# Kernel optimization log

Measured on AMD Instinct MI355X. Metric: run time of the kernel, lower is better.

Reference implementation:

```python
import jax, jax.numpy as jnp
import numpy as np

N = 50000
E = 600000
D = 128
BN_EPS = 1e-5


def _gcn_layer(x, src, dst, ew, W, b, n):
    # x: [N, Din] -> [N, Dout]; PyG GCNConv: linear, symmetric norm (self-loops
    # already appended to src/dst/ew by caller), gather, scatter-add, bias.
    h = x @ W  # [N, Dout]
    deg = jax.ops.segment_sum(ew, dst, num_segments=n)  # [N]
    dinv = jnp.where(deg > 0, jax.lax.rsqrt(jnp.maximum(deg, 1e-30)), 0.0)
    norm = dinv[src] * ew * dinv[dst]  # [E+N]
    msg = h[src] * norm[:, None]  # [E+N, Dout] -- dominant memory traffic
    out = jax.ops.segment_sum(msg, dst, num_segments=n)
    return out + b


def _bn_eval(x, gamma, beta, mean, var):
    return (x - mean) * jax.lax.rsqrt(var + BN_EPS) * gamma + beta


def setup_inputs() -> dict:
    key = jax.random.key(0)
    ks = jax.random.split(key, 16)
    s = 1.0 / np.sqrt(D)
    inp = {
        "x": jax.random.normal(ks[0], (N, D), dtype=jnp.float32),
        "edge_index": jax.random.randint(ks[1], (2, E), 0, N, dtype=jnp.int32),
        "edge_weight": jax.random.uniform(ks[2], (E,), dtype=jnp.float32),
        "W0": jax.random.uniform(ks[3], (D, D), jnp.float32, -s, s),
        "b0": jnp.zeros((D,), jnp.float32),
        "W1": jax.random.uniform(ks[4], (D, D), jnp.float32, -s, s),
        "b1": jnp.zeros((D,), jnp.float32),
        "gamma0": jnp.ones((D,), jnp.float32),
        "beta0": jnp.zeros((D,), jnp.float32),
        "mean0": 0.1 * jax.random.normal(ks[5], (D,), jnp.float32),
        "var0": jax.random.uniform(ks[6], (D,), jnp.float32, 0.5, 1.5),
        "gamma1": jnp.ones((D,), jnp.float32),
        "beta1": jnp.zeros((D,), jnp.float32),
        "mean1": 0.1 * jax.random.normal(ks[7], (D,), jnp.float32),
        "var1": jax.random.uniform(ks[8], (D,), jnp.float32, 0.5, 1.5),
        "act_params": jnp.ones((2,), jnp.float32),  # activation_params init = ones(num_layers)
    }
    return inp


def reference(x, edge_index, edge_weight, W0, b0, W1, b1, gamma0, beta0, mean0, var0, gamma1, beta1, mean1, var1, act_params):
    # Add self-loops with weight 1 (PyG gcn_norm fill_value=1), shared by both layers.
    loop = jnp.arange(N, dtype=edge_index.dtype)
    src = jnp.concatenate([edge_index[0], loop])
    dst = jnp.concatenate([edge_index[1], loop])
    ew = jnp.concatenate([edge_weight, jnp.ones((N,), edge_weight.dtype)])

    # layer 0: conv -> BN (eval: running stats) -> adaptive ReLU/GELU blend
    h = _gcn_layer(x, src, dst, ew, W0, b0, N)
    h = _bn_eval(h, gamma0, beta0, mean0, var0)
    alpha = jax.nn.sigmoid(act_params[0])
    h = alpha * jax.nn.relu(h) + (1.0 - alpha) * jax.nn.gelu(h, approximate=False)
    # dropout: identity in eval mode

    # layer 1 (last): conv -> BN, no activation/dropout
    h = _gcn_layer(h, src, dst, ew, W1, b1, N)
    h = _bn_eval(h, gamma1, beta1, mean1, var1)
    return h
```

## Files before the change

### kernel.cpp

```cpp
#include <hip/hip_runtime.h>
#include <hip/hip_fp16.h>
#include <math.h>
#include <type_traits>

#define D 128
#define BN_EPS 1e-5f
#define BCAP 64
#define FIX_SCALE 268435456.0f
#define FIX_INV   (1.0f / 268435456.0f)

typedef _Float16 half8 __attribute__((ext_vector_type(8)));
typedef float f32x4 __attribute__((ext_vector_type(4)));

__global__ void k_init(uint4* __restrict__ z, int n4,
                       const float* __restrict__ W0, const float* __restrict__ W1,
                       _Float16* __restrict__ p0, _Float16* __restrict__ p1, int Z) {
  if ((int)blockIdx.x < Z) {
    int i = blockIdx.x * 256 + threadIdx.x;
    if (i < n4) z[i] = make_uint4(0u, 0u, 0u, 0u);
    return;
  }
  const float* W = (blockIdx.x - Z) ? W1 : W0;
  _Float16* P = (blockIdx.x - Z) ? p1 : p0;
  for (int idx = threadIdx.x; idx < 32 * 64; idx += 256) {
    int ntks = idx >> 6;
    int lane = idx & 63;
    int nt = ntks >> 2, ks = ntks & 3;
    int kb = ks * 32 + (lane >> 4) * 8;
    int c = nt * 16 + (lane & 15);
#pragma unroll
    for (int i = 0; i < 8; ++i)
      P[(size_t)idx * 8 + i] = (_Float16)W[(size_t)(kb + i) * D + c];
  }
}

__global__ __launch_bounds__(256) void k_cnt_gemm0(const float* __restrict__ X,
                                                   const _Float16* __restrict__ Bp,
                                                   __half* __restrict__ H,
                                                   const int* __restrict__ dst,
                                                   const float* __restrict__ ew,
                                                   unsigned long long* cnt8,
                                                   int* __restrict__ rank,
                                                   int n, int e, int Gg) {
  if ((int)blockIdx.x >= Gg) {
    int base = ((int)blockIdx.x - Gg) * 2048 + threadIdx.x;
#pragma unroll
    for (int jj = 0; jj < 8; ++jj) {
      int i = base + jj * 256;
      if (i < e) {
        unsigned long long add = (1ull << 40) |
            (unsigned long long)(ew[i] * FIX_SCALE);
        unsigned long long old = atomicAdd(&cnt8[(size_t)dst[i] * 8], add);
        rank[i] = (int)(old >> 40);
      }
    }
    return;
  }

  const int lane = threadIdx.x & 63;
  const int wave = threadIdx.x >> 6;
  const int r0 = blockIdx.x * 64 + wave * 16;
  const int arow = r0 + (lane & 15);
  const int kbase = (lane >> 4) * 8;
  const bool av = arow < n;

  f32x4 acc[8];
#pragma unroll
  for (int t = 0; t < 8; ++t) acc[t] = (f32x4){0.f, 0.f, 0.f, 0.f};

#pragma unroll
  for (int ks = 0; ks < 4; ++ks) {
    half8 a;
    if (av) {
      const float* ap = X + (size_t)arow * D + ks * 32 + kbase;
      float4 f0 = *(const float4*)ap;
      float4 f1 = *(const float4*)(ap + 4);
      a[0] = (_Float16)f0.x; a[1] = (_Float16)f0.y;
      a[2] = (_Float16)f0.z; a[3] = (_Float16)f0.w;
      a[4] = (_Float16)f1.x; a[5] = (_Float16)f1.y;
      a[6] = (_Float16)f1.z; a[7] = (_Float16)f1.w;
    } else {
#pragma unroll
      for (int i = 0; i < 8; ++i) a[i] = (_Float16)0.f;
    }
#pragma unroll
    for (int nt = 0; nt < 8; ++nt) {
      half8 b = *(const half8*)(Bp + ((size_t)(nt * 4 + ks) * 64 + lane) * 8);
      acc[nt] = __builtin_amdgcn_mfma_f32_16x16x32_f16(a, b, acc[nt], 0, 0, 0);
    }
  }

  const int rbase = (lane >> 4) * 4;
  const int col = lane & 15;
#pragma unroll
  for (int nt = 0; nt < 8; ++nt) {
#pragma unroll
    for (int j = 0; j < 4; ++j) {
      int rr = r0 + rbase + j;
      if (rr < n) H[(size_t)rr * D + nt * 16 + col] = __float2half(acc[nt][j]);
    }
  }
}

__global__ void k_dinv2(const unsigned long long* __restrict__ cnt8,
                        int* __restrict__ cnt, float* __restrict__ dinv, int n) {
  int g = blockIdx.x * blockDim.x + threadIdx.x;
  if (g < n) {
    unsigned long long pv = cnt8[(size_t)g * 8];
    cnt[g] = (int)(pv >> 40);
    float ewsum = (float)(pv & 0xFFFFFFFFFFull) * FIX_INV;
    dinv[g] = rsqrtf(1.0f + ewsum);
  }
}

__global__ void k_bucket(const int* __restrict__ src, const int* __restrict__ dst,
                         const float* __restrict__ ew,
                         const int* __restrict__ rank, const float* __restrict__ dinv,
                         unsigned* __restrict__ pack4, int e) {
  int i = blockIdx.x * blockDim.x + threadIdx.x;
  if (i < e) {
    int d = dst[i], s = src[i];
    size_t pos = (size_t)d * BCAP + rank[i];
    __half c = __float2half(dinv[s] * ew[i]);
    pack4[pos] = ((unsigned)s << 16) | (unsigned)__half_as_ushort(c);
  }
}

__device__ __forceinline__ void h8_to_f(const uint4& r, float* f) {
  const __half2* hp = (const __half2*)&r;
#pragma unroll
  for (int t = 0; t < 4; ++t) {
    float2 v = __half22float2(hp[t]);
    f[2 * t] = v.x; f[2 * t + 1] = v.y;
  }
}

template <bool ACT>
__device__ __forceinline__ void agg_node(const __half* __restrict__ H,
                                         const unsigned* __restrict__ bkt, int kcnt,
                                         const float* __restrict__ dinv,
                                         const float* __restrict__ bias,
                                         const float* __restrict__ gamma,
                                         const float* __restrict__ beta,
                                         const float* __restrict__ mean,
                                         const float* __restrict__ var,
                                         float alpha, int g, int q, int j, float* acc) {
#pragma unroll
  for (int t = 0; t < 8; ++t) acc[t] = 0.f;

  for (int kb = 0; kb < kcnt; kb += 16) {
    int m = kcnt - kb;
    if (m > 16) m = 16;
    unsigned pl = 0u;
    if (q < m) pl = bkt[kb + q];
#pragma unroll
    for (int t = 0; t < 16; ++t) {
      if (t < m) {
        unsigned pp = (unsigned)__shfl((int)pl, t, 16);
        float w = __half2float(__ushort_as_half((unsigned short)(pp & 0xffffu)));
        uint4 r = *(const uint4*)(H + (size_t)(pp >> 16) * D + j);
        float f[8];
        h8_to_f(r, f);
#pragma unroll
        for (int u = 0; u < 8; ++u) acc[u] += w * f[u];
      }
    }
  }

  float dg = dinv[g];
  uint4 rs = *(const uint4*)(H + (size_t)g * D + j);
  float fs[8];
  h8_to_f(rs, fs);
#pragma unroll
  for (int t = 0; t < 8; ++t) acc[t] = dg * acc[t] + dg * dg * fs[t];

  float bb[8], gm[8], bt[8], mn[8], vr[8];
  *(float4*)&bb[0] = *(const float4*)(bias + j);  *(float4*)&bb[4] = *(const float4*)(bias + j + 4);
  *(float4*)&gm[0] = *(const float4*)(gamma + j); *(float4*)&gm[4] = *(const float4*)(gamma + j + 4);
  *(float4*)&bt[0] = *(const float4*)(beta + j);  *(float4*)&bt[4] = *(const float4*)(beta + j + 4);
  *(float4*)&mn[0] = *(const float4*)(mean + j);  *(float4*)&mn[4] = *(const float4*)(mean + j + 4);
  *(float4*)&vr[0] = *(const float4*)(var + j);   *(float4*)&vr[4] = *(const float4*)(var + j + 4);

#pragma unroll
  for (int t = 0; t < 8; ++t) {
    float vv = (acc[t] + bb[t] - mn[t]) * rsqrtf(vr[t] + BN_EPS) * gm[t] + bt[t];
    if (ACT) {
      float rl = fmaxf(vv, 0.f);
      float ge = 0.5f * vv * (1.f + erff(vv * 0.70710678118654752f));
      vv = alpha * rl + (1.f - alpha) * ge;
    }
    acc[t] = vv;
  }
}

__global__ __launch_bounds__(256) void k_agg_gemm(const __half* __restrict__ H,
                                                  const int* __restrict__ cnt,
                                                  const unsigned* __restrict__ pack4,
                                                  const float* __restrict__ dinv,
                                                  const float* __restrict__ bias,
                                                  const float* __restrict__ gamma,
                                                  const float* __restrict__ beta,
                                                  const float* __restrict__ mean,
                                                  const float* __restrict__ var,
                                                  const float* __restrict__ act_params,
                                                  const _Float16* __restrict__ Bp,
                                                  __half* __restrict__ Hout, int n) {
  __shared__ _Float16 sA[16][136];
  const int tid = threadIdx.x;
  const int row0 = blockIdx.x * 16;
  const int grp = tid >> 4;
  const int q = tid & 15;
  const int j = q * 8;
  const float alpha = 1.f / (1.f + expf(-act_params[0]));

  const int g = row0 + grp;
  half8 st;
  if (g < n) {
    float acc[8];
    agg_node<true>(H, pack4 + (size_t)g * BCAP, cnt[g], dinv,
                   bias, gamma, beta, mean, var, alpha, g, q, j, acc);
#pragma unroll
    for (int t = 0; t < 8; ++t) st[t] = (_Float16)acc[t];
  } else {
#pragma unroll
    for (int t = 0; t < 8; ++t) st[t] = (_Float16)0.f;
  }
  *(half8*)&sA[grp][j] = st;
  __syncthreads();

  const int lane = tid & 63;
  const int wave = tid >> 6;
  const int ntb = wave * 2;
  const int arowl = lane & 15;
  const int kbase = (lane >> 4) * 8;

  f32x4 acc[2];
#pragma unroll
  for (int t = 0; t < 2; ++t) acc[t] = (f32x4){0.f, 0.f, 0.f, 0.f};

#pragma unroll
  for (int ks = 0; ks < 4; ++ks) {
    half8 a = *(const half8*)&sA[arowl][ks * 32 + kbase];
#pragma unroll
    for (int nt = 0; nt < 2; ++nt) {
      half8 b = *(const half8*)(Bp + ((size_t)((ntb + nt) * 4 + ks) * 64 + lane) * 8);
      acc[nt] = __builtin_amdgcn_mfma_f32_16x16x32_f16(a, b, acc[nt], 0, 0, 0);
    }
  }

  const int rbase = (lane >> 4) * 4;
  const int col = lane & 15;
#pragma unroll
  for (int nt = 0; nt < 2; ++nt) {
#pragma unroll
    for (int jj = 0; jj < 4; ++jj) {
      int rr = row0 + rbase + jj;
      if (rr < n) Hout[(size_t)rr * D + (ntb + nt) * 16 + col] = __float2half(acc[nt][jj]);
    }
  }
}

template <typename OutT, bool ACT>
__global__ __launch_bounds__(256) void k_agg(const __half* __restrict__ H,
                                             const int* __restrict__ cnt,
                                             const unsigned* __restrict__ pack4,
                                             const float* __restrict__ dinv,
                                             const float* __restrict__ bias,
                                             const float* __restrict__ gamma,
                                             const float* __restrict__ beta,
                                             const float* __restrict__ mean,
                                             const float* __restrict__ var,
                                             const float* __restrict__ act_params,
                                             OutT* __restrict__ out, int n) {
  int g = blockIdx.x * 16 + (threadIdx.x >> 4);
  if (g >= n) return;
  const int q = threadIdx.x & 15;
  const int j = q * 8;
  const float alpha = ACT ? 1.f / (1.f + expf(-act_params[0])) : 0.f;

  float acc[8];
  agg_node<ACT>(H, pack4 + (size_t)g * BCAP, cnt[g], dinv,
                bias, gamma, beta, mean, var, alpha, g, q, j, acc);

  if constexpr (std::is_same<OutT, __half>::value) {
    uint4 st;
    __half2* hp = (__half2*)&st;
    hp[0] = __floats2half2_rn(acc[0], acc[1]);
    hp[1] = __floats2half2_rn(acc[2], acc[3]);
    hp[2] = __floats2half2_rn(acc[4], acc[5]);
    hp[3] = __floats2half2_rn(acc[6], acc[7]);
    *(uint4*)(out + (size_t)g * D + j) = st;
  } else {
    *(float4*)(out + (size_t)g * D + j)     = make_float4(acc[0], acc[1], acc[2], acc[3]);
    *(float4*)(out + (size_t)g * D + j + 4) = make_float4(acc[4], acc[5], acc[6], acc[7]);
  }
}

extern "C" void kernel_launch(void* const* d_in, const int* in_sizes, int n_in,
                              void* d_out, int out_size, void* d_ws, size_t ws_size,
                              hipStream_t stream) {
  const float* x      = (const float*)d_in[0];
  const int*   ei     = (const int*)d_in[1];
  const float* ew     = (const float*)d_in[2];
  const float* W0     = (const float*)d_in[3];
  const float* b0     = (const float*)d_in[4];
  const float* W1     = (const float*)d_in[5];
  const float* b1     = (const float*)d_in[6];
  const float* gamma0 = (const float*)d_in[7];
  const float* beta0  = (const float*)d_in[8];
  const float* mean0  = (const float*)d_in[9];
  const float* var0   = (const float*)d_in[10];
  const float* gamma1 = (const float*)d_in[11];
  const float* beta1  = (const float*)d_in[12];
  const float* mean1  = (const float*)d_in[13];
  const float* var1   = (const float*)d_in[14];
  const float* act    = (const float*)d_in[15];

  const int n = in_sizes[0] / D;
  const int e = in_sizes[2];
  const int* srcp = ei;
  const int* dstp = ei + e;

  uintptr_t p = (uintptr_t)d_ws;
  auto carve = [&p](size_t bytes) -> void* {
    void* r = (void*)p;
    p += (bytes + 255) & ~(size_t)255;
    return r;
  };
  float*    dinv  = (float*)carve(sizeof(float) * n);
  int*      cnt   = (int*)carve(sizeof(int) * n);
  int*      rank  = (int*)carve(sizeof(int) * e);
  unsigned long long* cnt8 = (unsigned long long*)carve(sizeof(unsigned long long) * (size_t)n * 8);
  _Float16* w0p   = (_Float16*)carve(sizeof(_Float16) * 32 * 64 * 8);
  _Float16* w1p   = (_Float16*)carve(sizeof(_Float16) * 32 * 64 * 8);
  unsigned* pack4 = (unsigned*)carve(sizeof(unsigned) * (size_t)n * BCAP);
  __half*   h16   = (__half*)carve(sizeof(__half) * (size_t)n * D);
  __half*   h16b  = (__half*)carve(sizeof(__half) * (size_t)n * D);
  float*    out   = (float*)d_out;

  const int tpb = 256;
  const int nb_n = (n + tpb - 1) / tpb;
  const int nb_e = (e + tpb - 1) / tpb;
  const int Gc   = (e + 2047) / 2048;
  const int Gg   = (n + 63) / 64;
  const int nz4  = n * 4;
  const int Z    = (nz4 + tpb - 1) / tpb;

  k_init<<<Z + 2, tpb, 0, stream>>>((uint4*)cnt8, nz4, W0, W1, w0p, w1p, Z);
  k_cnt_gemm0<<<Gg + Gc, tpb, 0, stream>>>(x, w0p, h16, dstp, ew, cnt8, rank, n, e, Gg);
  k_dinv2<<<nb_n, tpb, 0, stream>>>(cnt8, cnt, dinv, n);
  k_bucket<<<nb_e, tpb, 0, stream>>>(srcp, dstp, ew, rank, dinv, pack4, e);

  k_agg_gemm<<<(n + 15) / 16, tpb, 0, stream>>>(
      h16, cnt, pack4, dinv, b0, gamma0, beta0, mean0, var0, act, w1p, h16b, n);

  k_agg<float, false><<<(n + 15) / 16, tpb, 0, stream>>>(
      h16b, cnt, pack4, dinv, b1, gamma1, beta1, mean1, var1, act, out, n);
}
```

Measured before the change: 119.6 us.

## Fuse edge bucketing into the counting atomic pass, deferring dinv[src] to aggregation

Edges are now written directly into per-destination buckets at the moment the atomic counter returns their rank. This removes the separate bucket kernel and the rank array. Because dinv is not yet known at that point, each bucket entry becomes 8 bytes (src, fp32 edge weight), and dinv[src] is gathered inside both aggregation kernels. The trade is one fewer launch and less rank traffic, against twice the bucket bytes and an extra random dinv gather per edge in each of the two aggregations.

```diff
diff --git a/kernel.cpp b/kernel.cpp
--- a/kernel.cpp
+++ b/kernel.cpp
@@ -34,24 +34,29 @@
   }
 }
 
-__global__ __launch_bounds__(256) void k_cnt_gemm0(const float* __restrict__ X,
-                                                   const _Float16* __restrict__ Bp,
-                                                   __half* __restrict__ H,
-                                                   const int* __restrict__ dst,
-                                                   const float* __restrict__ ew,
-                                                   unsigned long long* cnt8,
-                                                   int* __restrict__ rank,
-                                                   int n, int e, int Gg) {
+__global__ __launch_bounds__(256) void k_scat_gemm0(const float* __restrict__ X,
+                                                    const _Float16* __restrict__ Bp,
+                                                    __half* __restrict__ H,
+                                                    const int* __restrict__ src,
+                                                    const int* __restrict__ dst,
+                                                    const float* __restrict__ ew,
+                                                    unsigned long long* cnt8,
+                                                    uint2* __restrict__ pack8,
+                                                    int n, int e, int Gg) {
   if ((int)blockIdx.x >= Gg) {
     int base = ((int)blockIdx.x - Gg) * 2048 + threadIdx.x;
 #pragma unroll
     for (int jj = 0; jj < 8; ++jj) {
       int i = base + jj * 256;
       if (i < e) {
+        float w = ew[i];
+        int d = dst[i];
         unsigned long long add = (1ull << 40) |
-            (unsigned long long)(ew[i] * FIX_SCALE);
-        unsigned long long old = atomicAdd(&cnt8[(size_t)dst[i] * 8], add);
-        rank[i] = (int)(old >> 40);
+            (unsigned long long)(w * FIX_SCALE);
+        unsigned long long old = atomicAdd(&cnt8[(size_t)d * 8], add);
+        int rank = (int)(old >> 40);
+        pack8[(size_t)d * BCAP + rank] =
+            make_uint2((unsigned)src[i], __float_as_uint(w));
       }
     }
     return;
@@ -113,19 +118,6 @@
   }
 }
 
-__global__ void k_bucket(const int* __restrict__ src, const int* __restrict__ dst,
-                         const float* __restrict__ ew,
-                         const int* __restrict__ rank, const float* __restrict__ dinv,
-                         unsigned* __restrict__ pack4, int e) {
-  int i = blockIdx.x * blockDim.x + threadIdx.x;
-  if (i < e) {
-    int d = dst[i], s = src[i];
-    size_t pos = (size_t)d * BCAP + rank[i];
-    __half c = __float2half(dinv[s] * ew[i]);
-    pack4[pos] = ((unsigned)s << 16) | (unsigned)__half_as_ushort(c);
-  }
-}
-
 __device__ __forceinline__ void h8_to_f(const uint4& r, float* f) {
   const __half2* hp = (const __half2*)&r;
 #pragma unroll
@@ -137,7 +129,7 @@
 
 template <bool ACT>
 __device__ __forceinline__ void agg_node(const __half* __restrict__ H,
-                                         const unsigned* __restrict__ bkt, int kcnt,
+                                         const uint2* __restrict__ bkt, int kcnt,
                                          const float* __restrict__ dinv,
                                          const float* __restrict__ bias,
                                          const float* __restrict__ gamma,
@@ -151,14 +143,19 @@
   for (int kb = 0; kb < kcnt; kb += 16) {
     int m = kcnt - kb;
     if (m > 16) m = 16;
-    unsigned pl = 0u;
-    if (q < m) pl = bkt[kb + q];
+    unsigned sl = 0u;
+    float wl = 0.f;
+    if (q < m) {
+      uint2 pl = bkt[kb + q];
+      sl = pl.x;
+      wl = dinv[pl.x] * __uint_as_float(pl.y);
+    }
 #pragma unroll
     for (int t = 0; t < 16; ++t) {
       if (t < m) {
-        unsigned pp = (unsigned)__shfl((int)pl, t, 16);
-        float w = __half2float(__ushort_as_half((unsigned short)(pp & 0xffffu)));
-        uint4 r = *(const uint4*)(H + (size_t)(pp >> 16) * D + j);
+        unsigned s = (unsigned)__shfl((int)sl, t, 16);
+        float w = __shfl(wl, t, 16);
+        uint4 r = *(const uint4*)(H + (size_t)s * D + j);
         float f[8];
         h8_to_f(r, f);
 #pragma unroll
@@ -195,7 +192,7 @@
 
 __global__ __launch_bounds__(256) void k_agg_gemm(const __half* __restrict__ H,
                                                   const int* __restrict__ cnt,
-                                                  const unsigned* __restrict__ pack4,
+                                                  const uint2* __restrict__ pack8,
                                                   const float* __restrict__ dinv,
                                                   const float* __restrict__ bias,
                                                   const float* __restrict__ gamma,
@@ -217,7 +214,7 @@
   half8 st;
   if (g < n) {
     float acc[8];
-    agg_node<true>(H, pack4 + (size_t)g * BCAP, cnt[g], dinv,
+    agg_node<true>(H, pack8 + (size_t)g * BCAP, cnt[g], dinv,
                    bias, gamma, beta, mean, var, alpha, g, q, j, acc);
 #pragma unroll
     for (int t = 0; t < 8; ++t) st[t] = (_Float16)acc[t];
@@ -263,7 +260,7 @@
 template <typename OutT, bool ACT>
 __global__ __launch_bounds__(256) void k_agg(const __half* __restrict__ H,
                                              const int* __restrict__ cnt,
-                                             const unsigned* __restrict__ pack4,
+                                             const uint2* __restrict__ pack8,
                                              const float* __restrict__ dinv,
                                              const float* __restrict__ bias,
                                              const float* __restrict__ gamma,
@@ -279,7 +276,7 @@
   const float alpha = ACT ? 1.f / (1.f + expf(-act_params[0])) : 0.f;
 
   float acc[8];
-  agg_node<ACT>(H, pack4 + (size_t)g * BCAP, cnt[g], dinv,
+  agg_node<ACT>(H, pack8 + (size_t)g * BCAP, cnt[g], dinv,
                 bias, gamma, beta, mean, var, alpha, g, q, j, acc);
 
   if constexpr (std::is_same<OutT, __half>::value) {
@@ -329,31 +326,28 @@
   };
   float*    dinv  = (float*)carve(sizeof(float) * n);
   int*      cnt   = (int*)carve(sizeof(int) * n);
-  int*      rank  = (int*)carve(sizeof(int) * e);
   unsigned long long* cnt8 = (unsigned long long*)carve(sizeof(unsigned long long) * (size_t)n * 8);
   _Float16* w0p   = (_Float16*)carve(sizeof(_Float16) * 32 * 64 * 8);
   _Float16* w1p   = (_Float16*)carve(sizeof(_Float16) * 32 * 64 * 8);
-  unsigned* pack4 = (unsigned*)carve(sizeof(unsigned) * (size_t)n * BCAP);
+  uint2*    pack8 = (uint2*)carve(sizeof(uint2) * (size_t)n * BCAP);
   __half*   h16   = (__half*)carve(sizeof(__half) * (size_t)n * D);
   __half*   h16b  = (__half*)carve(sizeof(__half) * (size_t)n * D);
   float*    out   = (float*)d_out;
 
   const int tpb = 256;
   const int nb_n = (n + tpb - 1) / tpb;
-  const int nb_e = (e + tpb - 1) / tpb;
   const int Gc   = (e + 2047) / 2048;
   const int Gg   = (n + 63) / 64;
   const int nz4  = n * 4;
   const int Z    = (nz4 + tpb - 1) / tpb;
 
   k_init<<<Z + 2, tpb, 0, stream>>>((uint4*)cnt8, nz4, W0, W1, w0p, w1p, Z);
-  k_cnt_gemm0<<<Gg + Gc, tpb, 0, stream>>>(x, w0p, h16, dstp, ew, cnt8, rank, n, e, Gg);
+  k_scat_gemm0<<<Gg + Gc, tpb, 0, stream>>>(x, w0p, h16, srcp, dstp, ew, cnt8, pack8, n, e, Gg);
   k_dinv2<<<nb_n, tpb, 0, stream>>>(cnt8, cnt, dinv, n);
-  k_bucket<<<nb_e, tpb, 0, stream>>>(srcp, dstp, ew, rank, dinv, pack4, e);
 
   k_agg_gemm<<<(n + 15) / 16, tpb, 0, stream>>>(
-      h16, cnt, pack4, dinv, b0, gamma0, beta0, mean0, var0, act, w1p, h16b, n);
+      h16, cnt, pack8, dinv, b0, gamma0, beta0, mean0, var0, act, w1p, h16b, n);
 
   k_agg<float, false><<<(n + 15) / 16, tpb, 0, stream>>>(
-      h16b, cnt, pack4, dinv, b1, gamma1, beta1, mean1, var1, act, out, n);
-}
+      h16b, cnt, pack8, dinv, b1, gamma1, beta1, mean1, var1, act, out, n);
+}
```

Measured after the change: 117.5 us. About the same (-1.8%).
